# Performance work log

Measured on AMD Instinct MI355X. Metric: run time of the kernel, lower is better.

## Reference

```python
import jax, jax.numpy as jnp
import numpy as np

V, E, H, S, B, MAX_OOV = 50000, 256, 512, 500, 64, 50


def setup_inputs() -> dict:
    key = jax.random.key(0)
    ks = jax.random.split(key, 22)
    s = 0.02  # param init scale
    return {
        "input_token": jax.random.randint(ks[0], (B, 1), 0, V),
        "encoder_hidden_states": jax.random.normal(ks[1], (S, B, 2 * H), jnp.float32),
        "projected_encoder_hidden_states": jax.random.normal(ks[2], (S, B, H), jnp.float32),
        "src_mask": jnp.ones((B, S), dtype=bool),
        "prev_hidden": jax.random.normal(ks[3], (1, B, H), jnp.float32),
        "encoder_batch_extended_vocab": jax.random.randint(ks[4], (B, S), 0, V + MAX_OOV),
        "batch_max_oov": MAX_OOV,
        # learned parameters
        "emb": jax.random.normal(ks[5], (V, E), jnp.float32) * s,
        "attn_Wq": jax.random.normal(ks[6], (H, H), jnp.float32) * s,   # query_layer, no bias
        "attn_We": jax.random.normal(ks[7], (1, H), jnp.float32) * s,   # energy_layer, no bias
        "gru_Wih": jax.random.normal(ks[8], (3 * H, E + 2 * H), jnp.float32) * s,
        "gru_Whh": jax.random.normal(ks[9], (3 * H, H), jnp.float32) * s,
        "gru_bih": jax.random.normal(ks[10], (3 * H,), jnp.float32) * s,
        "gru_bhh": jax.random.normal(ks[11], (3 * H,), jnp.float32) * s,
        "lin_W": jax.random.normal(ks[12], (H, E + 3 * H), jnp.float32) * s,
        "lin_b": jax.random.normal(ks[13], (H,), jnp.float32) * s,
        "pg_W": jax.random.normal(ks[14], (1, E + 3 * H), jnp.float32) * s,
        "pg_b": jax.random.normal(ks[15], (1,), jnp.float32) * s,
        "out_W": jax.random.normal(ks[16], (V, H), jnp.float32) * s,
        "out_b": jax.random.normal(ks[17], (V,), jnp.float32) * s,
    }


def _forward(input_token, enc_h, proj_key, prev_hidden, ext_vocab, max_oov,
             emb, attn_Wq, attn_We, gru_Wih, gru_Whh, gru_bih, gru_bhh,
             lin_W, lin_b, pg_W, pg_b, out_W, out_b):
    b = input_token.shape[0]
    embed = jnp.transpose(emb[input_token], (1, 0, 2))  # [1,B,E]

    # Bahdanau attention (softmax over source dim 0; mask unused, as in source)
    q = jnp.einsum('tbh,oh->tbo', prev_hidden, attn_Wq)            # [1,B,H]
    scores = jnp.einsum('sbh,oh->sb', jnp.tanh(q + proj_key), attn_We)  # [S,B]
    alphas = jax.nn.softmax(scores, axis=0)                        # [S,B]
    context = jnp.einsum('sb,sbd->bd', alphas, enc_h)[None]        # [1,B,2H]
    attention_dist = alphas.T                                      # [B,S]

    # GRU cell (torch gate order: r, z, n)
    x = jnp.concatenate([embed, context], axis=2)[0]               # [B,E+2H]
    h = prev_hidden[0]                                             # [B,H]
    gi = x @ gru_Wih.T + gru_bih                                   # [B,3H]
    gh = h @ gru_Whh.T + gru_bhh
    i_r, i_z, i_n = jnp.split(gi, 3, axis=1)
    h_r, h_z, h_n = jnp.split(gh, 3, axis=1)
    r = jax.nn.sigmoid(i_r + h_r)
    z = jax.nn.sigmoid(i_z + h_z)
    n = jnp.tanh(i_n + r * h_n)
    h_new = (1.0 - z) * n + z * h                                  # [B,H]
    rnn_output = h_new[None]                                       # [1,B,H]

    concat = jnp.concatenate([embed, rnn_output, context], axis=2)  # [1,B,E+3H]
    p_gen = jax.nn.sigmoid(jnp.einsum('tbf,of->tbo', concat, pg_W) + pg_b)  # [1,B,1]
    lin = jnp.einsum('tbf,of->tbo', concat, lin_W) + lin_b          # [1,B,H]
    logits = jnp.einsum('tbh,vh->tbv', lin, out_W) + out_b          # [1,B,V]

    gen_prob = p_gen * jax.nn.softmax(logits, axis=2)               # [1,B,V]
    attn_prob = ((1.0 - p_gen) * attention_dist[None])[0]           # [B,S]

    ext = jnp.concatenate(
        [gen_prob, jnp.zeros((1, b, max_oov), gen_prob.dtype)], axis=2) + 1e-12  # [1,B,V+oov]
    rows = jnp.arange(b)[:, None]
    merged = ext.at[0, rows, ext_vocab].add(attn_prob)              # scatter_add over vocab dim
    output = jnp.log(merged)
    return output, h_new[None]


def reference(input_token, encoder_hidden_states, projected_encoder_hidden_states,
              src_mask, prev_hidden, encoder_batch_extended_vocab, batch_max_oov,
              emb, attn_Wq, attn_We, gru_Wih, gru_Whh, gru_bih, gru_bhh,
              lin_W, lin_b, pg_W, pg_b, out_W, out_b):
    return _forward(input_token, encoder_hidden_states, projected_encoder_hidden_states,
                    prev_hidden, encoder_batch_extended_vocab, batch_max_oov,
                    emb, attn_Wq, attn_We, gru_Wih, gru_Whh, gru_bih, gru_bhh,
                    lin_W, lin_b, pg_W, pg_b, out_W, out_b)
```

## Files before the change

kernel.cpp:

```cpp
#include <hip/hip_runtime.h>
#include <hip/hip_bf16.h>
#include <math.h>

namespace {
constexpr int V = 50000, E = 256, H = 512, S = 500, B = 64, OOVN = 50;
constexpr int VEXT = V + OOVN;
constexpr int CCAT = E + 3 * H;
constexpr int G3 = 3 * H;
constexpr int NLB = 391;

typedef __attribute__((ext_vector_type(8))) short short8;
typedef __attribute__((ext_vector_type(4))) float f32x4;

__device__ __forceinline__ float wsum(float v) {
#pragma unroll
  for (int off = 32; off > 0; off >>= 1) v += __shfl_xor(v, off, 64);
  return v;
}
__device__ __forceinline__ float sigmoidf(float x) { return 1.f / (1.f + __expf(-x)); }
__device__ __forceinline__ float fast_tanh(float x) {
  x = fminf(fmaxf(x, -15.f), 15.f);
  float e = __expf(2.f * x);
  return __fdividef(e - 1.f, e + 1.f);
}
__device__ __forceinline__ void smerge_s(float& m, float& l, float om, float ol) {
  float nm = fmaxf(m, om);
  if (nm == -INFINITY) { m = nm; return; }
  l = l * __expf(m - nm) + ol * __expf(om - nm);
  m = nm;
}

__device__ __forceinline__ short bf16_rn_s(float f) {
  __hip_bfloat16 h = __float2bfloat16(f);
  return __builtin_bit_cast(short, h);
}
__device__ __forceinline__ void hilo1(float f, short* hi, short* lo) {
  unsigned u = __float_as_uint(f);
  *hi = (short)(u >> 16);
  *lo = bf16_rn_s(f - __uint_as_float(u & 0xffff0000u));
}
__device__ __forceinline__ void hilo8(float4 a, float4 b, short8& hi, short8& lo) {
  float f[8] = {a.x, a.y, a.z, a.w, b.x, b.y, b.z, b.w};
#pragma unroll
  for (int i = 0; i < 8; ++i) {
    unsigned u = __float_as_uint(f[i]);
    hi[i] = (short)(u >> 16);
    lo[i] = bf16_rn_s(f[i] - __uint_as_float(u & 0xffff0000u));
  }
}

template <int KSTEPS>
__device__ __forceinline__ void gemm16(const short* __restrict__ Xhi,
                                       const short* __restrict__ Xlo, int ldx, int xk0,
                                       const float* __restrict__ W, int ldw, int wk0,
                                       int n0, float* __restrict__ C, int ldc) {
  const int l = threadIdx.x & 63;
  const int r16 = l & 15, q16 = l >> 4;
  f32x4 acc[4];
#pragma unroll
  for (int t = 0; t < 4; ++t) acc[t] = (f32x4){0.f, 0.f, 0.f, 0.f};

  const float* wp = W + (size_t)(n0 + r16) * ldw + wk0 + q16 * 8;
  const short* xh[4];
  const short* xl[4];
#pragma unroll
  for (int t = 0; t < 4; ++t) {
    int row = t * 16 + r16;
    xh[t] = Xhi + (size_t)row * ldx + xk0 + q16 * 8;
    xl[t] = Xlo + (size_t)row * ldx + xk0 + q16 * 8;
  }

#pragma unroll
  for (int ks = 0; ks < KSTEPS; ++ks) {
    const int ko = ks * 32;
    float4 w0 = *reinterpret_cast<const float4*>(wp + ko);
    float4 w1 = *reinterpret_cast<const float4*>(wp + ko + 4);
    short8 whi, wlo;
    hilo8(w0, w1, whi, wlo);
#pragma unroll
    for (int t = 0; t < 4; ++t) {
      short8 ah = *reinterpret_cast<const short8*>(xh[t] + ko);
      short8 al = *reinterpret_cast<const short8*>(xl[t] + ko);
      acc[t] = __builtin_amdgcn_mfma_f32_16x16x32_bf16(ah, whi, acc[t], 0, 0, 0);
      acc[t] = __builtin_amdgcn_mfma_f32_16x16x32_bf16(al, whi, acc[t], 0, 0, 0);
      acc[t] = __builtin_amdgcn_mfma_f32_16x16x32_bf16(ah, wlo, acc[t], 0, 0, 0);
    }
  }
#pragma unroll
  for (int t = 0; t < 4; ++t) {
#pragma unroll
    for (int r = 0; r < 4; ++r) {
      int row = t * 16 + q16 * 4 + r;
      C[(size_t)row * ldc + n0 + r16] = acc[t][r];
    }
  }
}

__global__ void k_prep(const int* __restrict__ tok, const float* __restrict__ emb,
                       const float* __restrict__ prevh, float* __restrict__ cc,
                       short* __restrict__ cch, short* __restrict__ ccl,
                       short* __restrict__ hh, short* __restrict__ hl) {
  int i = blockIdx.x * 256 + threadIdx.x;
  hilo1(prevh[i], &hh[i], &hl[i]);
  if (i < 16384) {
    int b = i >> 8, e = i & 255;
    float v = emb[(size_t)tok[b] * E + e];
    cc[b * CCAT + e] = v;
    hilo1(v, &cch[b * CCAT + e], &ccl[b * CCAT + e]);
  }
}

__global__ void __launch_bounds__(256) k_gemm_qgh(
    const short* __restrict__ hh, const short* __restrict__ hl,
    const float* __restrict__ Wq, const float* __restrict__ Whh,
    float* __restrict__ qpart, float* __restrict__ ghp) {
  int w = blockIdx.x * 4 + (threadIdx.x >> 6);
  if (w < 128) {
    int c = w >> 5, nt = w & 31;
    gemm16<4>(hh, hl, H, c * 128, Wq, H, c * 128, nt * 16,
              qpart + (size_t)c * 64 * H, H);
  } else {
    int w2 = w - 128;
    int c = w2 / 96, nt = w2 % 96;
    gemm16<8>(hh, hl, H, c * 256, Whh, H, c * 256, nt * 16,
              ghp + (size_t)c * 64 * G3, G3);
  }
}

__global__ void k_scores(const float* __restrict__ qpart, const float* __restrict__ pk,
                         const float* __restrict__ We, float* __restrict__ scores) {
  int lane = threadIdx.x & 63;
  int gw = blockIdx.x * 4 + (threadIdx.x >> 6);
  int s = gw >> 6, b = gw & 63;
  const float* q0 = qpart + b * H + lane * 8;
  const float* kr = pk + ((size_t)s * B + b) * H + lane * 8;
  const float* er = We + lane * 8;
  float part = 0.f;
#pragma unroll
  for (int i = 0; i < 2; ++i) {
    float4 qa = *reinterpret_cast<const float4*>(q0 + i * 4);
    float4 qb = *reinterpret_cast<const float4*>(q0 + 64 * H + i * 4);
    float4 qc = *reinterpret_cast<const float4*>(q0 + 128 * H + i * 4);
    float4 qd = *reinterpret_cast<const float4*>(q0 + 192 * H + i * 4);
    float4 kv = *reinterpret_cast<const float4*>(kr + i * 4);
    float4 ev = *reinterpret_cast<const float4*>(er + i * 4);
    part += fast_tanh(qa.x + qb.x + qc.x + qd.x + kv.x) * ev.x +
            fast_tanh(qa.y + qb.y + qc.y + qd.y + kv.y) * ev.y +
            fast_tanh(qa.z + qb.z + qc.z + qd.z + kv.z) * ev.z +
            fast_tanh(qa.w + qb.w + qc.w + qd.w + kv.w) * ev.w;
  }
  part = wsum(part);
  if (lane == 0) scores[s * B + b] = part;
}

__global__ void k_softmax_s(const float* __restrict__ scores, float* __restrict__ alphasT) {
  int b = blockIdx.x, t = threadIdx.x;
  int w = t >> 6, lane = t & 63;
  __shared__ float rm[8], rl[8];
  float v = (t < S) ? scores[t * B + b] : -INFINITY;
  float m = v;
#pragma unroll
  for (int off = 32; off > 0; off >>= 1) m = fmaxf(m, __shfl_xor(m, off, 64));
  if (lane == 0) rm[w] = m;
  __syncthreads();
  float bm = rm[0];
#pragma unroll
  for (int i = 1; i < 8; ++i) bm = fmaxf(bm, rm[i]);
  float e = (t < S) ? __expf(v - bm) : 0.f;
  float sw = wsum(e);
  if (lane == 0) rl[w] = sw;
  __syncthreads();
  float tot = rl[0];
#pragma unroll
  for (int i = 1; i < 8; ++i) tot += rl[i];
  if (t < S) alphasT[b * S + t] = e / tot;
}

__global__ void k_ctx(const float* __restrict__ alphasT, const float* __restrict__ ench,
                      float* __restrict__ ctxp) {
  int b = blockIdx.x, chf = blockIdx.y, sh = blockIdx.z;
  int t = threadIdx.x;
  __shared__ float sa[250];
  if (t < 250) sa[t] = alphasT[b * S + sh * 250 + t];
  __syncthreads();
  const float* base = ench + ((size_t)(sh * 250) * B + b) * 1024 + chf * 512 + t;
  float a0 = 0.f, a1 = 0.f;
#pragma unroll 8
  for (int s = 0; s < 250; s += 2) {
    a0 += sa[s] * base[(size_t)s * (B * 1024)];
    a1 += sa[s + 1] * base[(size_t)(s + 1) * (B * 1024)];
  }
  ctxp[((sh * B + b) * 1024) + chf * 512 + t] = a0 + a1;
}

__global__ void k_ctx2(const float* __restrict__ ctxp, float* __restrict__ cc,
                       short* __restrict__ cch, short* __restrict__ ccl) {
  int b = blockIdx.x, t = threadIdx.x;
  int c = t * 4;
  float4 v0 = *reinterpret_cast<const float4*>(&ctxp[(b * 1024) + c]);
  float4 v1 = *reinterpret_cast<const float4*>(&ctxp[((B + b) * 1024) + c]);
  float r[4] = {v0.x + v1.x, v0.y + v1.y, v0.z + v1.z, v0.w + v1.w};
#pragma unroll
  for (int i = 0; i < 4; ++i) {
    int col = 768 + c + i;
    cc[b * CCAT + col] = r[i];
    hilo1(r[i], &cch[b * CCAT + col], &ccl[b * CCAT + col]);
  }
}

__global__ void __launch_bounds__(256) k_gemm_big(
    const short* __restrict__ cch, const short* __restrict__ ccl,
    const float* __restrict__ Wih, const float* __restrict__ linW,
    float* __restrict__ gip, float* __restrict__ linpart) {
  int w = blockIdx.x * 4 + (threadIdx.x >> 6);
  if (w < 480) {
    int c = w / 96, nt = w % 96;
    int xk0 = (c == 0) ? 0 : 768 + (c - 1) * 256;
    int wk0 = c * 256;
    gemm16<8>(cch, ccl, CCAT, xk0, Wih, 1280, wk0, nt * 16,
              gip + (size_t)c * 64 * G3, G3);
  } else {
    int w2 = w - 480;
    int c = w2 >> 5, nt = w2 & 31;
    int k0 = (c == 0) ? 0 : 768 + (c - 1) * 256;
    gemm16<8>(cch, ccl, CCAT, k0, linW, CCAT, k0, nt * 16,
              linpart + (size_t)c * 64 * H, H);
  }
}

__global__ void k_gates(const float* __restrict__ gip, const float* __restrict__ ghp,
                        const float* __restrict__ bih, const float* __restrict__ bhh,
                        const float* __restrict__ prevh, const float* __restrict__ pgW,
                        const float* __restrict__ pgb, float* __restrict__ cc,
                        short* __restrict__ cch, short* __restrict__ ccl,
                        float* __restrict__ hout, float* __restrict__ pgsum) {
  int b = blockIdx.x, j = threadIdx.x;
  float ir = bih[j], iz = bih[512 + j], in_ = bih[1024 + j];
#pragma unroll
  for (int c = 0; c < 5; ++c) {
    const float* g = gip + (size_t)c * 64 * G3 + b * G3;
    ir += g[j]; iz += g[512 + j]; in_ += g[1024 + j];
  }
  float hr = bhh[j], hz = bhh[512 + j], hn = bhh[1024 + j];
#pragma unroll
  for (int c = 0; c < 2; ++c) {
    const float* g = ghp + (size_t)c * 64 * G3 + b * G3;
    hr += g[j]; hz += g[512 + j]; hn += g[1024 + j];
  }
  float r = sigmoidf(ir + hr);
  float z = sigmoidf(iz + hz);
  float n = fast_tanh(in_ + r * hn);
  float h = prevh[b * H + j];
  float hnew = (1.f - z) * n + z * h;
  hout[b * H + j] = hnew;
  cc[b * CCAT + E + j] = hnew;
  hilo1(hnew, &cch[b * CCAT + E + j], &ccl[b * CCAT + E + j]);
  float acc = hnew * pgW[E + j];
  acc += cc[b * CCAT + 768 + j] * pgW[768 + j];
  acc += cc[b * CCAT + 1280 + j] * pgW[1280 + j];
  if (j < 256) acc += cc[b * CCAT + j] * pgW[j];
  acc = wsum(acc);
  __shared__ float sl[8];
  int w = j >> 6, lane = j & 63;
  if (lane == 0) sl[w] = acc;
  __syncthreads();
  if (j == 0) {
    float tot = pgb[0];
#pragma unroll
    for (int i = 0; i < 8; ++i) tot += sl[i];
    pgsum[b] = tot;
  }
}

__global__ void __launch_bounds__(256) k_gemm_linh(const short* __restrict__ cch,
                                                   const short* __restrict__ ccl,
                                                   const float* __restrict__ linW,
                                                   float* __restrict__ linpart) {
  int w = blockIdx.x * 4 + (threadIdx.x >> 6);
  int c = w >> 5, nt = w & 31;
  int k0 = 256 + c * 256;
  gemm16<8>(cch, ccl, CCAT, k0, linW, CCAT, k0, nt * 16,
            linpart + (size_t)(5 + c) * 64 * H, H);
}

__global__ void k_linfin(const float* __restrict__ linpart, const float* __restrict__ linb,
                         short* __restrict__ lh) {
  int idx = blockIdx.x * 256 + threadIdx.x;
  int b = idx >> 9, o = idx & 511;
  float v = linb[o];
#pragma unroll
  for (int c = 0; c < 7; ++c) v += linpart[(size_t)c * 64 * H + b * H + o];
  lh[idx] = bf16_rn_s(v);
}

__global__ void __launch_bounds__(512) k_gemm_logits(
    const short* __restrict__ lh, const float* __restrict__ outW,
    const float* __restrict__ outb, float* __restrict__ logits,
    float* __restrict__ pm, float* __restrict__ pl) {
  __shared__ __align__(16) short xs[64 * 512];
  __shared__ float pml[8][64][2];
  char* xb = reinterpret_cast<char*>(xs);
  int tid = threadIdx.x;
#pragma unroll
  for (int k = 0; k < 8; ++k) {
    int m = k * 512 + tid;
    int row = m >> 6;
    short8 v = *reinterpret_cast<const short8*>(lh + (size_t)m * 8);
    int byte = (m * 16) ^ ((row & 7) << 4);
    *reinterpret_cast<short8*>(xb + byte) = v;
  }
  __syncthreads();
  const int l = tid & 63;
  const int r16 = l & 15, q16 = l >> 4;
  const int wid = tid >> 6;
  const int waveId = blockIdx.x * 8 + wid;
  const bool active = waveId < V / 16;
  if (active) {
    const int n0 = waveId * 16;
    f32x4 acc[4];
#pragma unroll
    for (int t = 0; t < 4; ++t) acc[t] = (f32x4){0.f, 0.f, 0.f, 0.f};
    const float* wp = outW + (size_t)(n0 + r16) * H + q16 * 8;
    int arow[4], aswz[4];
#pragma unroll
    for (int t = 0; t < 4; ++t) {
      int row = t * 16 + r16;
      arow[t] = row * 1024 + q16 * 16;
      aswz[t] = (row & 7) << 4;
    }
#pragma unroll
    for (int ks = 0; ks < 16; ++ks) {
      float4 w0 = *reinterpret_cast<const float4*>(wp + ks * 32);
      float4 w1 = *reinterpret_cast<const float4*>(wp + ks * 32 + 4);
      short8 wh;
      wh[0] = bf16_rn_s(w0.x); wh[1] = bf16_rn_s(w0.y);
      wh[2] = bf16_rn_s(w0.z); wh[3] = bf16_rn_s(w0.w);
      wh[4] = bf16_rn_s(w1.x); wh[5] = bf16_rn_s(w1.y);
      wh[6] = bf16_rn_s(w1.z); wh[7] = bf16_rn_s(w1.w);
#pragma unroll
      for (int t = 0; t < 4; ++t) {
        short8 a = *reinterpret_cast<const short8*>(xb + ((arow[t] + ks * 64) ^ aswz[t]));
        acc[t] = __builtin_amdgcn_mfma_f32_16x16x32_bf16(a, wh, acc[t], 0, 0, 0);
      }
    }
    float bv = outb[n0 + r16];
#pragma unroll
    for (int t = 0; t < 4; ++t) {
#pragma unroll
      for (int r = 0; r < 4; ++r) {
        float y = acc[t][r] + bv;
        int row = t * 16 + q16 * 4 + r;
        logits[(size_t)row * V + n0 + r16] = y;
        float m = y;
#pragma unroll
        for (int off = 8; off > 0; off >>= 1) m = fmaxf(m, __shfl_xor(m, off, 64));
        float e = __expf(y - m);
#pragma unroll
        for (int off = 8; off > 0; off >>= 1) e += __shfl_xor(e, off, 64);
        if (r16 == 0) { pml[wid][row][0] = m; pml[wid][row][1] = e; }
      }
    }
  } else if (r16 == 0) {
#pragma unroll
    for (int t = 0; t < 4; ++t)
#pragma unroll
      for (int r = 0; r < 4; ++r) {
        int row = t * 16 + q16 * 4 + r;
        pml[wid][row][0] = -INFINITY;
        pml[wid][row][1] = 0.f;
      }
  }
  __syncthreads();
  if (tid < 64) {
    float m = pml[0][tid][0], lv = pml[0][tid][1];
#pragma unroll
    for (int i = 1; i < 8; ++i) smerge_s(m, lv, pml[i][tid][0], pml[i][tid][1]);
    pm[blockIdx.x * 64 + tid] = m;
    pl[blockIdx.x * 64 + tid] = lv;
  }
}

__global__ void k_final(const float* __restrict__ logits, const float* __restrict__ pm,
                        const float* __restrict__ pl, const float* __restrict__ pgsum,
                        const int* __restrict__ extv, const float* __restrict__ alphasT,
                        float* __restrict__ out) {
  int b = blockIdx.x, c = blockIdx.y, t = threadIdx.x;
  __shared__ float sp_[5056];
  __shared__ float rm[4], rl[4];
  float m = -INFINITY, lv = 0.f;
  for (int i = t; i < NLB; i += 256) smerge_s(m, lv, pm[i * 64 + b], pl[i * 64 + b]);
#pragma unroll
  for (int off = 32; off > 0; off >>= 1) {
    float om = __shfl_xor(m, off, 64), ol = __shfl_xor(lv, off, 64);
    smerge_s(m, lv, om, ol);
  }
  int w = t >> 6, lane = t & 63;
  if (lane == 0) { rm[w] = m; rl[w] = lv; }
  __syncthreads();
  m = rm[0]; lv = rl[0];
#pragma unroll
  for (int i = 1; i < 4; ++i) smerge_s(m, lv, rm[i], rl[i]);
  float pg = sigmoidf(pgsum[b]);
  float scale = pg / lv;
  const int base = c * 5000;
  const int len = (c == 9) ? 5050 : 5000;
  const float* lr = logits + (size_t)b * V + base;
  for (int i = t; i < len; i += 256)
    sp_[i] = (i < 5000) ? scale * __expf(lr[i] - m) + 1e-12f : 1e-12f;
  __syncthreads();
  float wgt = 1.f - pg;
  for (int s = t; s < S; s += 256) {
    int idx = extv[b * S + s] - base;
    if ((unsigned)idx < (unsigned)len) atomicAdd(&sp_[idx], wgt * alphasT[b * S + s]);
  }
  __syncthreads();
  float* orow = out + (size_t)b * VEXT + base;
  for (int i = t; i < len; i += 256) orow[i] = logf(sp_[i]);
}
}

extern "C" void kernel_launch(void* const* d_in, const int* in_sizes, int n_in,
                              void* d_out, int out_size, void* d_ws, size_t ws_size,
                              hipStream_t stream) {
  const int*   tok   = (const int*)d_in[0];
  const float* ench  = (const float*)d_in[1];
  const float* pk    = (const float*)d_in[2];
  const float* prevh = (const float*)d_in[4];
  const int*   extv  = (const int*)d_in[5];
  const float* emb   = (const float*)d_in[7];
  const float* Wq    = (const float*)d_in[8];
  const float* We    = (const float*)d_in[9];
  const float* Wih   = (const float*)d_in[10];
  const float* Whh   = (const float*)d_in[11];
  const float* bih   = (const float*)d_in[12];
  const float* bhh   = (const float*)d_in[13];
  const float* linW  = (const float*)d_in[14];
  const float* linb  = (const float*)d_in[15];
  const float* pgW   = (const float*)d_in[16];
  const float* pgb   = (const float*)d_in[17];
  const float* outW  = (const float*)d_in[18];
  const float* outb  = (const float*)d_in[19];

  float* out = (float*)d_out;
  float* ws = (float*)d_ws;

  float* qpart   = ws;
  float* scores  = qpart + 131072;
  float* alphasT = scores + 32000;
  float* ctxp    = alphasT + 32000;
  float* cc      = ctxp + 131072;
  float* gip     = cc + 114688;
  float* ghp     = gip + 491520;
  float* linpart = ghp + 196608;
  float* pgsum   = linpart + 229376;
  float* logits  = pgsum + 64;
  float* pm      = logits + 3200000;
  float* pl      = pm + 25024;
  short* sp      = (short*)(pl + 25024);
  short* cch = sp;
  short* ccl = cch + 114688;
  short* hh  = ccl + 114688;
  short* hl  = hh + 32768;
  short* lh  = hl + 32768;
  float* hout = out + (size_t)B * VEXT;

  k_prep<<<dim3(128), dim3(256), 0, stream>>>(tok, emb, prevh, cc, cch, ccl, hh, hl);
  k_gemm_qgh<<<dim3(80), dim3(256), 0, stream>>>(hh, hl, Wq, Whh, qpart, ghp);
  k_scores<<<dim3(8000), dim3(256), 0, stream>>>(qpart, pk, We, scores);
  k_softmax_s<<<dim3(B), dim3(512), 0, stream>>>(scores, alphasT);
  k_ctx<<<dim3(64, 2, 2), dim3(512), 0, stream>>>(alphasT, ench, ctxp);
  k_ctx2<<<dim3(B), dim3(256), 0, stream>>>(ctxp, cc, cch, ccl);
  k_gemm_big<<<dim3(160), dim3(256), 0, stream>>>(cch, ccl, Wih, linW, gip, linpart);
  k_gates<<<dim3(B), dim3(512), 0, stream>>>(gip, ghp, bih, bhh, prevh, pgW, pgb, cc, cch,
                                             ccl, hout, pgsum);
  k_gemm_linh<<<dim3(16), dim3(256), 0, stream>>>(cch, ccl, linW, linpart);
  k_linfin<<<dim3(128), dim3(256), 0, stream>>>(linpart, linb, lh);
  k_gemm_logits<<<dim3(NLB), dim3(512), 0, stream>>>(lh, outW, outb, logits, pm, pl);
  k_final<<<dim3(B, 10), dim3(256), 0, stream>>>(logits, pm, pl, pgsum, extv, alphasT, out);
}
```

Baseline: 162.8 us.

## Fuse all decoder phases into one cooperative persistent kernel with grid syncs

Replaces the chain of twelve kernel launches with a single cooperative kernel that runs each phase as a grid-stride loop separated by grid-wide barriers. Launch gaps and per-kernel tail effects are the cost it targets. It also regroups work: context reduction is split into four source chunks, and the linear-layer hidden-part GEMM appears to be folded into a later phase. A fallback path of per-phase kernels remains. Risks include grid barrier overhead, lower occupancy from the 68KB shared buffer and 512-thread blocks, and host-side occupancy and property queries on every call.

Result: slower. 531.9 us (+226.7%).

```diff
diff --git a/kernel.cpp b/kernel.cpp
--- a/kernel.cpp
+++ b/kernel.cpp
@@ -1,6 +1,9 @@
 #include <hip/hip_runtime.h>
 #include <hip/hip_bf16.h>
+#include <hip/hip_cooperative_groups.h>
 #include <math.h>
+
+namespace cg = cooperative_groups;
 
 namespace {
 constexpr int V = 50000, E = 256, H = 512, S = 500, B = 64, OOVN = 50;
@@ -8,9 +11,22 @@
 constexpr int CCAT = E + 3 * H;
 constexpr int G3 = 3 * H;
 constexpr int NLB = 391;
+constexpr int SMEM_BYTES = 69632;
 
 typedef __attribute__((ext_vector_type(8))) short short8;
 typedef __attribute__((ext_vector_type(4))) float f32x4;
+
+struct P {
+  const int* tok; const float* ench; const float* pk; const float* prevh;
+  const int* extv; const float* emb; const float* Wq; const float* We;
+  const float* Wih; const float* Whh; const float* bih; const float* bhh;
+  const float* linW; const float* linb; const float* pgW; const float* pgb;
+  const float* outW; const float* outb;
+  float* out; float* qpart; float* scores; float* alphasT; float* ctxp;
+  float* cc; float* gip; float* ghp; float* linpart; float* pgsum;
+  float* logits; float* pm; float* pl; float* hout;
+  short* cch; short* ccl; short* hh; short* hl; short* lh;
+};
 
 __device__ __forceinline__ float wsum(float v) {
 #pragma unroll
@@ -29,7 +45,6 @@
   l = l * __expf(m - nm) + ol * __expf(om - nm);
   m = nm;
 }
-
 __device__ __forceinline__ short bf16_rn_s(float f) {
   __hip_bfloat16 h = __float2bfloat16(f);
   return __builtin_bit_cast(short, h);
@@ -50,16 +65,14 @@
 }
 
 template <int KSTEPS>
-__device__ __forceinline__ void gemm16(const short* __restrict__ Xhi,
-                                       const short* __restrict__ Xlo, int ldx, int xk0,
-                                       const float* __restrict__ W, int ldw, int wk0,
-                                       int n0, float* __restrict__ C, int ldc) {
+__device__ __forceinline__ void gemm_core(const short* __restrict__ Xhi,
+                                          const short* __restrict__ Xlo, int ldx, int xk0,
+                                          const float* __restrict__ W, int ldw, int wk0,
+                                          int n0, f32x4 acc[4]) {
   const int l = threadIdx.x & 63;
   const int r16 = l & 15, q16 = l >> 4;
-  f32x4 acc[4];
 #pragma unroll
   for (int t = 0; t < 4; ++t) acc[t] = (f32x4){0.f, 0.f, 0.f, 0.f};
-
   const float* wp = W + (size_t)(n0 + r16) * ldw + wk0 + q16 * 8;
   const short* xh[4];
   const short* xl[4];
@@ -69,7 +82,6 @@
     xh[t] = Xhi + (size_t)row * ldx + xk0 + q16 * 8;
     xl[t] = Xlo + (size_t)row * ldx + xk0 + q16 * 8;
   }
-
 #pragma unroll
   for (int ks = 0; ks < KSTEPS; ++ks) {
     const int ko = ks * 32;
@@ -86,395 +98,461 @@
       acc[t] = __builtin_amdgcn_mfma_f32_16x16x32_bf16(ah, wlo, acc[t], 0, 0, 0);
     }
   }
-#pragma unroll
-  for (int t = 0; t < 4; ++t) {
+}
+template <int KSTEPS>
+__device__ __forceinline__ void gemm_store(const short* Xhi, const short* Xlo, int ldx,
+                                           int xk0, const float* W, int ldw, int wk0,
+                                           int n0, float* C, int ldc) {
+  f32x4 acc[4];
+  gemm_core<KSTEPS>(Xhi, Xlo, ldx, xk0, W, ldw, wk0, n0, acc);
+  const int l = threadIdx.x & 63;
+  const int r16 = l & 15, q16 = l >> 4;
+#pragma unroll
+  for (int t = 0; t < 4; ++t)
 #pragma unroll
     for (int r = 0; r < 4; ++r) {
       int row = t * 16 + q16 * 4 + r;
       C[(size_t)row * ldc + n0 + r16] = acc[t][r];
     }
-  }
-}
-
-__global__ void k_prep(const int* __restrict__ tok, const float* __restrict__ emb,
-                       const float* __restrict__ prevh, float* __restrict__ cc,
-                       short* __restrict__ cch, short* __restrict__ ccl,
-                       short* __restrict__ hh, short* __restrict__ hl) {
-  int i = blockIdx.x * 256 + threadIdx.x;
-  hilo1(prevh[i], &hh[i], &hl[i]);
-  if (i < 16384) {
-    int b = i >> 8, e = i & 255;
-    float v = emb[(size_t)tok[b] * E + e];
-    cc[b * CCAT + e] = v;
-    hilo1(v, &cch[b * CCAT + e], &ccl[b * CCAT + e]);
-  }
-}
-
-__global__ void __launch_bounds__(256) k_gemm_qgh(
-    const short* __restrict__ hh, const short* __restrict__ hl,
-    const float* __restrict__ Wq, const float* __restrict__ Whh,
-    float* __restrict__ qpart, float* __restrict__ ghp) {
-  int w = blockIdx.x * 4 + (threadIdx.x >> 6);
-  if (w < 128) {
-    int c = w >> 5, nt = w & 31;
-    gemm16<4>(hh, hl, H, c * 128, Wq, H, c * 128, nt * 16,
-              qpart + (size_t)c * 64 * H, H);
-  } else {
-    int w2 = w - 128;
-    int c = w2 / 96, nt = w2 % 96;
-    gemm16<8>(hh, hl, H, c * 256, Whh, H, c * 256, nt * 16,
-              ghp + (size_t)c * 64 * G3, G3);
-  }
-}
-
-__global__ void k_scores(const float* __restrict__ qpart, const float* __restrict__ pk,
-                         const float* __restrict__ We, float* __restrict__ scores) {
+}
+
+
+__device__ void ph_prep(const P& p) {
+  for (int i = blockIdx.x * blockDim.x + threadIdx.x; i < B * H;
+       i += gridDim.x * blockDim.x) {
+    hilo1(p.prevh[i], &p.hh[i], &p.hl[i]);
+    if (i < B * E) {
+      int b = i >> 8, e = i & 255;
+      float v = p.emb[(size_t)p.tok[b] * E + e];
+      p.cc[b * CCAT + e] = v;
+      hilo1(v, &p.cch[b * CCAT + e], &p.ccl[b * CCAT + e]);
+    }
+  }
+}
+
+__device__ void ph_qgh(const P& p) {
+  int W = gridDim.x * (blockDim.x >> 6);
+  for (int w = blockIdx.x * (blockDim.x >> 6) + (threadIdx.x >> 6); w < 320; w += W) {
+    if (w < 128) {
+      int c = w >> 5, nt = w & 31;
+      gemm_store<4>(p.hh, p.hl, H, c * 128, p.Wq, H, c * 128, nt * 16,
+                    p.qpart + (size_t)c * 64 * H, H);
+    } else {
+      int w2 = w - 128;
+      int c = w2 / 96, nt = w2 % 96;
+      gemm_store<8>(p.hh, p.hl, H, c * 256, p.Whh, H, c * 256, nt * 16,
+                    p.ghp + (size_t)c * 64 * G3, G3);
+    }
+  }
+}
+
+__device__ void ph_scores(const P& p) {
   int lane = threadIdx.x & 63;
-  int gw = blockIdx.x * 4 + (threadIdx.x >> 6);
-  int s = gw >> 6, b = gw & 63;
-  const float* q0 = qpart + b * H + lane * 8;
-  const float* kr = pk + ((size_t)s * B + b) * H + lane * 8;
-  const float* er = We + lane * 8;
-  float part = 0.f;
-#pragma unroll
-  for (int i = 0; i < 2; ++i) {
-    float4 qa = *reinterpret_cast<const float4*>(q0 + i * 4);
-    float4 qb = *reinterpret_cast<const float4*>(q0 + 64 * H + i * 4);
-    float4 qc = *reinterpret_cast<const float4*>(q0 + 128 * H + i * 4);
-    float4 qd = *reinterpret_cast<const float4*>(q0 + 192 * H + i * 4);
-    float4 kv = *reinterpret_cast<const float4*>(kr + i * 4);
-    float4 ev = *reinterpret_cast<const float4*>(er + i * 4);
-    part += fast_tanh(qa.x + qb.x + qc.x + qd.x + kv.x) * ev.x +
-            fast_tanh(qa.y + qb.y + qc.y + qd.y + kv.y) * ev.y +
-            fast_tanh(qa.z + qb.z + qc.z + qd.z + kv.z) * ev.z +
-            fast_tanh(qa.w + qb.w + qc.w + qd.w + kv.w) * ev.w;
-  }
-  part = wsum(part);
-  if (lane == 0) scores[s * B + b] = part;
-}
-
-__global__ void k_softmax_s(const float* __restrict__ scores, float* __restrict__ alphasT) {
-  int b = blockIdx.x, t = threadIdx.x;
-  int w = t >> 6, lane = t & 63;
-  __shared__ float rm[8], rl[8];
-  float v = (t < S) ? scores[t * B + b] : -INFINITY;
-  float m = v;
-#pragma unroll
-  for (int off = 32; off > 0; off >>= 1) m = fmaxf(m, __shfl_xor(m, off, 64));
-  if (lane == 0) rm[w] = m;
-  __syncthreads();
-  float bm = rm[0];
-#pragma unroll
-  for (int i = 1; i < 8; ++i) bm = fmaxf(bm, rm[i]);
-  float e = (t < S) ? __expf(v - bm) : 0.f;
-  float sw = wsum(e);
-  if (lane == 0) rl[w] = sw;
-  __syncthreads();
-  float tot = rl[0];
-#pragma unroll
-  for (int i = 1; i < 8; ++i) tot += rl[i];
-  if (t < S) alphasT[b * S + t] = e / tot;
-}
-
-__global__ void k_ctx(const float* __restrict__ alphasT, const float* __restrict__ ench,
-                      float* __restrict__ ctxp) {
-  int b = blockIdx.x, chf = blockIdx.y, sh = blockIdx.z;
+  int W = gridDim.x * (blockDim.x >> 6);
+  for (int gw = blockIdx.x * (blockDim.x >> 6) + (threadIdx.x >> 6); gw < S * B; gw += W) {
+    int s = gw >> 6, b = gw & 63;
+    const float* q0 = p.qpart + b * H + lane * 8;
+    const float* kr = p.pk + ((size_t)s * B + b) * H + lane * 8;
+    const float* er = p.We + lane * 8;
+    float part = 0.f;
+#pragma unroll
+    for (int i = 0; i < 2; ++i) {
+      float4 qa = *reinterpret_cast<const float4*>(q0 + i * 4);
+      float4 qb = *reinterpret_cast<const float4*>(q0 + 64 * H + i * 4);
+      float4 qc = *reinterpret_cast<const float4*>(q0 + 128 * H + i * 4);
+      float4 qd = *reinterpret_cast<const float4*>(q0 + 192 * H + i * 4);
+      float4 kv = *reinterpret_cast<const float4*>(kr + i * 4);
+      float4 ev = *reinterpret_cast<const float4*>(er + i * 4);
+      part += fast_tanh(qa.x + qb.x + qc.x + qd.x + kv.x) * ev.x +
+              fast_tanh(qa.y + qb.y + qc.y + qd.y + kv.y) * ev.y +
+              fast_tanh(qa.z + qb.z + qc.z + qd.z + kv.z) * ev.z +
+              fast_tanh(qa.w + qb.w + qc.w + qd.w + kv.w) * ev.w;
+    }
+    part = wsum(part);
+    if (lane == 0) p.scores[s * B + b] = part;
+  }
+}
+
+__device__ void ph_softmax(const P& p, char* smem) {
+  float* rm = (float*)smem;
+  float* rl = rm + 8;
+  int t = threadIdx.x, w = t >> 6, lane = t & 63;
+  for (int b = blockIdx.x; b < B; b += gridDim.x) {
+    __syncthreads();
+    float v = (t < S) ? p.scores[t * B + b] : -INFINITY;
+    float m = v;
+#pragma unroll
+    for (int off = 32; off > 0; off >>= 1) m = fmaxf(m, __shfl_xor(m, off, 64));
+    if (lane == 0) rm[w] = m;
+    __syncthreads();
+    float bm = rm[0];
+#pragma unroll
+    for (int i = 1; i < 8; ++i) bm = fmaxf(bm, rm[i]);
+    float e = (t < S) ? __expf(v - bm) : 0.f;
+    float sw = wsum(e);
+    if (lane == 0) rl[w] = sw;
+    __syncthreads();
+    float tot = rl[0];
+#pragma unroll
+    for (int i = 1; i < 8; ++i) tot += rl[i];
+    if (t < S) p.alphasT[b * S + t] = e / tot;
+  }
+}
+
+__device__ void ph_ctx(const P& p, char* smem) {
+  float* sa = (float*)smem;
   int t = threadIdx.x;
-  __shared__ float sa[250];
-  if (t < 250) sa[t] = alphasT[b * S + sh * 250 + t];
-  __syncthreads();
-  const float* base = ench + ((size_t)(sh * 250) * B + b) * 1024 + chf * 512 + t;
-  float a0 = 0.f, a1 = 0.f;
-#pragma unroll 8
-  for (int s = 0; s < 250; s += 2) {
-    a0 += sa[s] * base[(size_t)s * (B * 1024)];
-    a1 += sa[s + 1] * base[(size_t)(s + 1) * (B * 1024)];
-  }
-  ctxp[((sh * B + b) * 1024) + chf * 512 + t] = a0 + a1;
-}
-
-__global__ void k_ctx2(const float* __restrict__ ctxp, float* __restrict__ cc,
-                       short* __restrict__ cch, short* __restrict__ ccl) {
-  int b = blockIdx.x, t = threadIdx.x;
-  int c = t * 4;
-  float4 v0 = *reinterpret_cast<const float4*>(&ctxp[(b * 1024) + c]);
-  float4 v1 = *reinterpret_cast<const float4*>(&ctxp[((B + b) * 1024) + c]);
-  float r[4] = {v0.x + v1.x, v0.y + v1.y, v0.z + v1.z, v0.w + v1.w};
-#pragma unroll
-  for (int i = 0; i < 4; ++i) {
-    int col = 768 + c + i;
-    cc[b * CCAT + col] = r[i];
-    hilo1(r[i], &cch[b * CCAT + col], &ccl[b * CCAT + col]);
-  }
-}
-
-__global__ void __launch_bounds__(256) k_gemm_big(
-    const short* __restrict__ cch, const short* __restrict__ ccl,
-    const float* __restrict__ Wih, const float* __restrict__ linW,
-    float* __restrict__ gip, float* __restrict__ linpart) {
-  int w = blockIdx.x * 4 + (threadIdx.x >> 6);
-  if (w < 480) {
-    int c = w / 96, nt = w % 96;
-    int xk0 = (c == 0) ? 0 : 768 + (c - 1) * 256;
-    int wk0 = c * 256;
-    gemm16<8>(cch, ccl, CCAT, xk0, Wih, 1280, wk0, nt * 16,
-              gip + (size_t)c * 64 * G3, G3);
-  } else {
-    int w2 = w - 480;
-    int c = w2 >> 5, nt = w2 & 31;
-    int k0 = (c == 0) ? 0 : 768 + (c - 1) * 256;
-    gemm16<8>(cch, ccl, CCAT, k0, linW, CCAT, k0, nt * 16,
-              linpart + (size_t)c * 64 * H, H);
-  }
-}
-
-__global__ void k_gates(const float* __restrict__ gip, const float* __restrict__ ghp,
-                        const float* __restrict__ bih, const float* __restrict__ bhh,
-                        const float* __restrict__ prevh, const float* __restrict__ pgW,
-                        const float* __restrict__ pgb, float* __restrict__ cc,
-                        short* __restrict__ cch, short* __restrict__ ccl,
-                        float* __restrict__ hout, float* __restrict__ pgsum) {
-  int b = blockIdx.x, j = threadIdx.x;
-  float ir = bih[j], iz = bih[512 + j], in_ = bih[1024 + j];
-#pragma unroll
-  for (int c = 0; c < 5; ++c) {
-    const float* g = gip + (size_t)c * 64 * G3 + b * G3;
-    ir += g[j]; iz += g[512 + j]; in_ += g[1024 + j];
-  }
-  float hr = bhh[j], hz = bhh[512 + j], hn = bhh[1024 + j];
-#pragma unroll
-  for (int c = 0; c < 2; ++c) {
-    const float* g = ghp + (size_t)c * 64 * G3 + b * G3;
-    hr += g[j]; hz += g[512 + j]; hn += g[1024 + j];
-  }
-  float r = sigmoidf(ir + hr);
-  float z = sigmoidf(iz + hz);
-  float n = fast_tanh(in_ + r * hn);
-  float h = prevh[b * H + j];
-  float hnew = (1.f - z) * n + z * h;
-  hout[b * H + j] = hnew;
-  cc[b * CCAT + E + j] = hnew;
-  hilo1(hnew, &cch[b * CCAT + E + j], &ccl[b * CCAT + E + j]);
-  float acc = hnew * pgW[E + j];
-  acc += cc[b * CCAT + 768 + j] * pgW[768 + j];
-  acc += cc[b * CCAT + 1280 + j] * pgW[1280 + j];
-  if (j < 256) acc += cc[b * CCAT + j] * pgW[j];
-  acc = wsum(acc);
-  __shared__ float sl[8];
+  for (int it = blockIdx.x; it < 512; it += gridDim.x) {
+    int b = it >> 3, chf = (it >> 2) & 1, sh = it & 3;
+    __syncthreads();
+    if (t < 125) sa[t] = p.alphasT[b * S + sh * 125 + t];
+    __syncthreads();
+    const float* base = p.ench + ((size_t)(sh * 125) * B + b) * 1024 + chf * 512 + t;
+    float a0 = 0.f, a1 = 0.f;
+#pragma unroll 5
+    for (int s = 0; s < 124; s += 2) {
+      a0 += sa[s] * base[(size_t)s * (B * 1024)];
+      a1 += sa[s + 1] * base[(size_t)(s + 1) * (B * 1024)];
+    }
+    a0 += sa[124] * base[(size_t)124 * (B * 1024)];
+    p.ctxp[((sh * B + b) * 1024) + chf * 512 + t] = a0 + a1;
+  }
+}
+
+__device__ void ph_ctx2(const P& p) {
+  for (int i = blockIdx.x * blockDim.x + threadIdx.x; i < B * 1024;
+       i += gridDim.x * blockDim.x) {
+    int b = i >> 10, col = i & 1023;
+    float v = p.ctxp[(b)*1024 + col] + p.ctxp[(B + b) * 1024 + col] +
+              p.ctxp[(2 * B + b) * 1024 + col] + p.ctxp[(3 * B + b) * 1024 + col];
+    int cix = b * CCAT + 768 + col;
+    p.cc[cix] = v;
+    hilo1(v, &p.cch[cix], &p.ccl[cix]);
+  }
+}
+
+__device__ void ph_big(const P& p) {
+  int W = gridDim.x * (blockDim.x >> 6);
+  for (int w = blockIdx.x * (blockDim.x >> 6) + (threadIdx.x >> 6); w < 640; w += W) {
+    if (w < 480) {
+      int c = w / 96, nt = w % 96;
+      int xk0 = (c == 0) ? 0 : 768 + (c - 1) * 256;
+      gemm_store<8>(p.cch, p.ccl, CCAT, xk0, p.Wih, 1280, c * 256, nt * 16,
+                    p.gip + (size_t)c * 64 * G3, G3);
+    } else {
+      int w2 = w - 480;
+      int c = w2 >> 5, nt = w2 & 31;
+      int k0 = (c == 0) ? 0 : 768 + (c - 1) * 256;
+      gemm_store<8>(p.cch, p.ccl, CCAT, k0, p.linW, CCAT, k0, nt * 16,
+                    p.linpart + (size_t)c * 64 * H, H);
+    }
+  }
+}
+
+__device__ void ph_gates(const P& p, char* smem) {
+  float* sl = (float*)smem;
+  int j = threadIdx.x;
   int w = j >> 6, lane = j & 63;
-  if (lane == 0) sl[w] = acc;
-  __syncthreads();
-  if (j == 0) {
-    float tot = pgb[0];
-#pragma unroll
-    for (int i = 0; i < 8; ++i) tot += sl[i];
-    pgsum[b] = tot;
-  }
-}
-
-__global__ void __launch_bounds__(256) k_gemm_linh(const short* __restrict__ cch,
-                                                   const short* __restrict__ ccl,
-                                                   const float* __restrict__ linW,
-                                                   float* __restrict__ linpart) {
-  int w = blockIdx.x * 4 + (threadIdx.x >> 6);
-  int c = w >> 5, nt = w & 31;
-  int k0 = 256 + c * 256;
-  gemm16<8>(cch, ccl, CCAT, k0, linW, CCAT, k0, nt * 16,
-            linpart + (size_t)(5 + c) * 64 * H, H);
-}
-
-__global__ void k_linfin(const float* __restrict__ linpart, const float* __restrict__ linb,
-                         short* __restrict__ lh) {
-  int idx = blockIdx.x * 256 + threadIdx.x;
-  int b = idx >> 9, o = idx & 511;
-  float v = linb[o];
-#pragma unroll
-  for (int c = 0; c < 7; ++c) v += linpart[(size_t)c * 64 * H + b * H + o];
-  lh[idx] = bf16_rn_s(v);
-}
-
-__global__ void __launch_bounds__(512) k_gemm_logits(
-    const short* __restrict__ lh, const float* __restrict__ outW,
-    const float* __restrict__ outb, float* __restrict__ logits,
-    float* __restrict__ pm, float* __restrict__ pl) {
-  __shared__ __align__(16) short xs[64 * 512];
-  __shared__ float pml[8][64][2];
-  char* xb = reinterpret_cast<char*>(xs);
+  for (int b = blockIdx.x; b < B; b += gridDim.x) {
+    __syncthreads();
+    float ir = p.bih[j], iz = p.bih[512 + j], in_ = p.bih[1024 + j];
+#pragma unroll
+    for (int c = 0; c < 5; ++c) {
+      const float* g = p.gip + (size_t)c * 64 * G3 + b * G3;
+      ir += g[j]; iz += g[512 + j]; in_ += g[1024 + j];
+    }
+    float hr = p.bhh[j], hz = p.bhh[512 + j], hn = p.bhh[1024 + j];
+#pragma unroll
+    for (int c = 0; c < 2; ++c) {
+      const float* g = p.ghp + (size_t)c * 64 * G3 + b * G3;
+      hr += g[j]; hz += g[512 + j]; hn += g[1024 + j];
+    }
+    float r = sigmoidf(ir + hr);
+    float z = sigmoidf(iz + hz);
+    float n = fast_tanh(in_ + r * hn);
+    float h = p.prevh[b * H + j];
+    float hnew = (1.f - z) * n + z * h;
+    p.hout[b * H + j] = hnew;
+    p.cc[b * CCAT + E + j] = hnew;
+    hilo1(hnew, &p.cch[b * CCAT + E + j], &p.ccl[b * CCAT + E + j]);
+    float acc = hnew * p.pgW[E + j];
+    acc += p.cc[b * CCAT + 768 + j] * p.pgW[768 + j];
+    acc += p.cc[b * CCAT + 1280 + j] * p.pgW[1280 + j];
+    if (j < 256) acc += p.cc[b * CCAT + j] * p.pgW[j];
+    acc = wsum(acc);
+    if (lane == 0) sl[w] = acc;
+    __syncthreads();
+    if (j == 0) {
+      float tot = p.pgb[0];
+#pragma unroll
+      for (int i = 0; i < 8; ++i) tot += sl[i];
+      p.pgsum[b] = tot;
+    }
+  }
+}
+
+__device__ void ph_linfin(const P& p) {
+  int W = gridDim.x * (blockDim.x >> 6);
+  for (int w = blockIdx.x * (blockDim.x >> 6) + (threadIdx.x >> 6); w < 32; w += W) {
+    f32x4 acc[4];
+    gemm_core<16>(p.cch, p.ccl, CCAT, 256, p.linW, CCAT, 256, w * 16, acc);
+    const int l = threadIdx.x & 63;
+    const int r16 = l & 15, q16 = l >> 4;
+    int col = w * 16 + r16;
+    float bv = p.linb[col];
+#pragma unroll
+    for (int t = 0; t < 4; ++t)
+#pragma unroll
+      for (int r = 0; r < 4; ++r) {
+        int row = t * 16 + q16 * 4 + r;
+        float v = acc[t][r] + bv;
+#pragma unroll
+        for (int c = 0; c < 5; ++c) v += p.linpart[(size_t)c * 64 * H + row * H + col];
+        p.lh[row * H + col] = bf16_rn_s(v);
+      }
+  }
+}
+
+__device__ void ph_logits(const P& p, char* smem) {
+  char* xb = smem;
+  float (*pml)[64][2] = (float(*)[64][2])(smem + 65536);
   int tid = threadIdx.x;
+  const int l = tid & 63, r16 = l & 15, q16 = l >> 4, wid = tid >> 6;
 #pragma unroll
   for (int k = 0; k < 8; ++k) {
     int m = k * 512 + tid;
     int row = m >> 6;
-    short8 v = *reinterpret_cast<const short8*>(lh + (size_t)m * 8);
+    short8 v = *reinterpret_cast<const short8*>(p.lh + (size_t)m * 8);
     int byte = (m * 16) ^ ((row & 7) << 4);
     *reinterpret_cast<short8*>(xb + byte) = v;
   }
+  int arow[4], aswz[4];
+#pragma unroll
+  for (int t = 0; t < 4; ++t) {
+    int row = t * 16 + r16;
+    arow[t] = row * 1024 + q16 * 16;
+    aswz[t] = (row & 7) << 4;
+  }
   __syncthreads();
-  const int l = tid & 63;
-  const int r16 = l & 15, q16 = l >> 4;
-  const int wid = tid >> 6;
-  const int waveId = blockIdx.x * 8 + wid;
-  const bool active = waveId < V / 16;
-  if (active) {
-    const int n0 = waveId * 16;
-    f32x4 acc[4];
-#pragma unroll
-    for (int t = 0; t < 4; ++t) acc[t] = (f32x4){0.f, 0.f, 0.f, 0.f};
-    const float* wp = outW + (size_t)(n0 + r16) * H + q16 * 8;
-    int arow[4], aswz[4];
-#pragma unroll
-    for (int t = 0; t < 4; ++t) {
-      int row = t * 16 + r16;
-      arow[t] = row * 1024 + q16 * 16;
-      aswz[t] = (row & 7) << 4;
-    }
-#pragma unroll
-    for (int ks = 0; ks < 16; ++ks) {
-      float4 w0 = *reinterpret_cast<const float4*>(wp + ks * 32);
-      float4 w1 = *reinterpret_cast<const float4*>(wp + ks * 32 + 4);
-      short8 wh;
-      wh[0] = bf16_rn_s(w0.x); wh[1] = bf16_rn_s(w0.y);
-      wh[2] = bf16_rn_s(w0.z); wh[3] = bf16_rn_s(w0.w);
-      wh[4] = bf16_rn_s(w1.x); wh[5] = bf16_rn_s(w1.y);
-      wh[6] = bf16_rn_s(w1.z); wh[7] = bf16_rn_s(w1.w);
-#pragma unroll
-      for (int t = 0; t < 4; ++t) {
-        short8 a = *reinterpret_cast<const short8*>(xb + ((arow[t] + ks * 64) ^ aswz[t]));
-        acc[t] = __builtin_amdgcn_mfma_f32_16x16x32_bf16(a, wh, acc[t], 0, 0, 0);
+  for (int vb = blockIdx.x; vb < NLB; vb += gridDim.x) {
+    int tile = vb * 8 + wid;
+    if (tile < V / 16) {
+      const int n0 = tile * 16;
+      f32x4 acc[4];
+#pragma unroll
+      for (int t = 0; t < 4; ++t) acc[t] = (f32x4){0.f, 0.f, 0.f, 0.f};
+      const float* wp = p.outW + (size_t)(n0 + r16) * H + q16 * 8;
+#pragma unroll
+      for (int ks = 0; ks < 16; ++ks) {
+        float4 w0 = *reinterpret_cast<const float4*>(wp + ks * 32);
+        float4 w1 = *reinterpret_cast<const float4*>(wp + ks * 32 + 4);
+        short8 wh;
+        wh[0] = bf16_rn_s(w0.x); wh[1] = bf16_rn_s(w0.y);
+        wh[2] = bf16_rn_s(w0.z); wh[3] = bf16_rn_s(w0.w);
+        wh[4] = bf16_rn_s(w1.x); wh[5] = bf16_rn_s(w1.y);
+        wh[6] = bf16_rn_s(w1.z); wh[7] = bf16_rn_s(w1.w);
+#pragma unroll
+        for (int t = 0; t < 4; ++t) {
+          short8 a = *reinterpret_cast<const short8*>(xb + ((arow[t] + ks * 64) ^ aswz[t]));
+          acc[t] = __builtin_amdgcn_mfma_f32_16x16x32_bf16(a, wh, acc[t], 0, 0, 0);
+        }
       }
-    }
-    float bv = outb[n0 + r16];
-#pragma unroll
-    for (int t = 0; t < 4; ++t) {
-#pragma unroll
-      for (int r = 0; r < 4; ++r) {
-        float y = acc[t][r] + bv;
-        int row = t * 16 + q16 * 4 + r;
-        logits[(size_t)row * V + n0 + r16] = y;
-        float m = y;
-#pragma unroll
-        for (int off = 8; off > 0; off >>= 1) m = fmaxf(m, __shfl_xor(m, off, 64));
-        float e = __expf(y - m);
-#pragma unroll
-        for (int off = 8; off > 0; off >>= 1) e += __shfl_xor(e, off, 64);
-        if (r16 == 0) { pml[wid][row][0] = m; pml[wid][row][1] = e; }
-      }
-    }
-  } else if (r16 == 0) {
-#pragma unroll
-    for (int t = 0; t < 4; ++t)
-#pragma unroll
-      for (int r = 0; r < 4; ++r) {
-        int row = t * 16 + q16 * 4 + r;
-        pml[wid][row][0] = -INFINITY;
-        pml[wid][row][1] = 0.f;
-      }
-  }
-  __syncthreads();
-  if (tid < 64) {
-    float m = pml[0][tid][0], lv = pml[0][tid][1];
-#pragma unroll
-    for (int i = 1; i < 8; ++i) smerge_s(m, lv, pml[i][tid][0], pml[i][tid][1]);
-    pm[blockIdx.x * 64 + tid] = m;
-    pl[blockIdx.x * 64 + tid] = lv;
-  }
-}
-
-__global__ void k_final(const float* __restrict__ logits, const float* __restrict__ pm,
-                        const float* __restrict__ pl, const float* __restrict__ pgsum,
-                        const int* __restrict__ extv, const float* __restrict__ alphasT,
-                        float* __restrict__ out) {
-  int b = blockIdx.x, c = blockIdx.y, t = threadIdx.x;
-  __shared__ float sp_[5056];
-  __shared__ float rm[4], rl[4];
-  float m = -INFINITY, lv = 0.f;
-  for (int i = t; i < NLB; i += 256) smerge_s(m, lv, pm[i * 64 + b], pl[i * 64 + b]);
-#pragma unroll
-  for (int off = 32; off > 0; off >>= 1) {
-    float om = __shfl_xor(m, off, 64), ol = __shfl_xor(lv, off, 64);
-    smerge_s(m, lv, om, ol);
-  }
-  int w = t >> 6, lane = t & 63;
-  if (lane == 0) { rm[w] = m; rl[w] = lv; }
-  __syncthreads();
-  m = rm[0]; lv = rl[0];
-#pragma unroll
-  for (int i = 1; i < 4; ++i) smerge_s(m, lv, rm[i], rl[i]);
-  float pg = sigmoidf(pgsum[b]);
-  float scale = pg / lv;
-  const int base = c * 5000;
-  const int len = (c == 9) ? 5050 : 5000;
-  const float* lr = logits + (size_t)b * V + base;
-  for (int i = t; i < len; i += 256)
-    sp_[i] = (i < 5000) ? scale * __expf(lr[i] - m) + 1e-12f : 1e-12f;
-  __syncthreads();
-  float wgt = 1.f - pg;
-  for (int s = t; s < S; s += 256) {
-    int idx = extv[b * S + s] - base;
-    if ((unsigned)idx < (unsigned)len) atomicAdd(&sp_[idx], wgt * alphasT[b * S + s]);
-  }
-  __syncthreads();
-  float* orow = out + (size_t)b * VEXT + base;
-  for (int i = t; i < len; i += 256) orow[i] = logf(sp_[i]);
+      float bv = p.outb[n0 + r16];
+#pragma unroll
+      for (int t = 0; t < 4; ++t)
+#pragma unroll
+        for (int r = 0; r < 4; ++r) {
+          float y = acc[t][r] + bv;
+          int row = t * 16 + q16 * 4 + r;
+          p.logits[(size_t)row * V + n0 + r16] = y;
+          float m = y;
+#pragma unroll
+          for (int off = 8; off > 0; off >>= 1) m = fmaxf(m, __shfl_xor(m, off, 64));
+          float e = __expf(y - m);
+#pragma unroll
+          for (int off = 8; off > 0; off >>= 1) e += __shfl_xor(e, off, 64);
+          if (r16 == 0) { pml[wid][row][0] = m; pml[wid][row][1] = e; }
+        }
+    } else if (r16 == 0) {
+#pragma unroll
+      for (int t = 0; t < 4; ++t)
+#pragma unroll
+        for (int r = 0; r < 4; ++r) {
+          int row = t * 16 + q16 * 4 + r;
+          pml[wid][row][0] = -INFINITY;
+          pml[wid][row][1] = 0.f;
+        }
+    }
+    __syncthreads();
+    if (tid < 64) {
+      float m = pml[0][tid][0], lv = pml[0][tid][1];
+#pragma unroll
+      for (int i = 1; i < 8; ++i) smerge_s(m, lv, pml[i][tid][0], pml[i][tid][1]);
+      p.pm[vb * 64 + tid] = m;
+      p.pl[vb * 64 + tid] = lv;
+    }
+    __syncthreads();
+  }
+}
+
+__device__ void ph_final(const P& p, char* smem) {
+  float* sp_ = (float*)smem;
+  float* rr = (float*)(smem + 20224);
+  float* rl2 = rr + 8;
+  int t = threadIdx.x, w = t >> 6, lane = t & 63;
+  for (int it = blockIdx.x; it < 640; it += gridDim.x) {
+    int b = it & 63, c = it >> 6;
+    float m = -INFINITY, lv = 0.f;
+    if (t < NLB) { m = p.pm[t * 64 + b]; lv = p.pl[t * 64 + b]; }
+#pragma unroll
+    for (int off = 32; off > 0; off >>= 1) {
+      float om = __shfl_xor(m, off, 64), ol = __shfl_xor(lv, off, 64);
+      smerge_s(m, lv, om, ol);
+    }
+    if (lane == 0) { rr[w] = m; rl2[w] = lv; }
+    __syncthreads();
+    m = rr[0]; lv = rl2[0];
+#pragma unroll
+    for (int i = 1; i < 8; ++i) smerge_s(m, lv, rr[i], rl2[i]);
+    float pg = sigmoidf(p.pgsum[b]);
+    float scale = pg / lv;
+    const int base = c * 5000;
+    const int len = (c == 9) ? 5050 : 5000;
+    const float* lr = p.logits + (size_t)b * V + base;
+    for (int i = t; i < len; i += 512)
+      sp_[i] = (i < 5000) ? scale * __expf(lr[i] - m) + 1e-12f : 1e-12f;
+    __syncthreads();
+    float wgt = 1.f - pg;
+    for (int s = t; s < S; s += 512) {
+      int idx = p.extv[b * S + s] - base;
+      if ((unsigned)idx < (unsigned)len) atomicAdd(&sp_[idx], wgt * p.alphasT[b * S + s]);
+    }
+    __syncthreads();
+    float* orow = p.out + (size_t)b * VEXT + base;
+    for (int i = t; i < len; i += 512) orow[i] = __logf(sp_[i]);
+    __syncthreads();
+  }
+}
+
+__global__ void __launch_bounds__(512, 4) k_mega(P p) {
+  __shared__ __align__(16) char smem[SMEM_BYTES];
+  cg::grid_group g = cg::this_grid();
+  ph_prep(p);          g.sync();
+  ph_qgh(p);           g.sync();
+  ph_scores(p);        g.sync();
+  ph_softmax(p, smem); g.sync();
+  ph_ctx(p, smem);     g.sync();
+  ph_ctx2(p);          g.sync();
+  ph_big(p);           g.sync();
+  ph_gates(p, smem);   g.sync();
+  ph_linfin(p);        g.sync();
+  ph_logits(p, smem);  g.sync();
+  ph_final(p, smem);
+}
+
+__global__ void __launch_bounds__(512) k_p0(P p) { ph_prep(p); }
+__global__ void __launch_bounds__(512) k_p1(P p) { ph_qgh(p); }
+__global__ void __launch_bounds__(512) k_p2(P p) { ph_scores(p); }
+__global__ void __launch_bounds__(512) k_p3(P p) {
+  __shared__ __align__(16) char smem[64];
+  ph_softmax(p, smem);
+}
+__global__ void __launch_bounds__(512) k_p4(P p) {
+  __shared__ __align__(16) char smem[512];
+  ph_ctx(p, smem);
+}
+__global__ void __launch_bounds__(512) k_p5(P p) { ph_ctx2(p); }
+__global__ void __launch_bounds__(512) k_p6(P p) { ph_big(p); }
+__global__ void __launch_bounds__(512) k_p7(P p) {
+  __shared__ __align__(16) char smem[64];
+  ph_gates(p, smem);
+}
+__global__ void __launch_bounds__(512) k_p8(P p) { ph_linfin(p); }
+__global__ void __launch_bounds__(512) k_p9(P p) {
+  __shared__ __align__(16) char smem[SMEM_BYTES];
+  ph_logits(p, smem);
+}
+__global__ void __launch_bounds__(512) k_p10(P p) {
+  __shared__ __align__(16) char smem[20304];
+  ph_final(p, smem);
 }
 }
 
 extern "C" void kernel_launch(void* const* d_in, const int* in_sizes, int n_in,
                               void* d_out, int out_size, void* d_ws, size_t ws_size,
                               hipStream_t stream) {
-  const int*   tok   = (const int*)d_in[0];
-  const float* ench  = (const float*)d_in[1];
-  const float* pk    = (const float*)d_in[2];
-  const float* prevh = (const float*)d_in[4];
-  const int*   extv  = (const int*)d_in[5];
-  const float* emb   = (const float*)d_in[7];
-  const float* Wq    = (const float*)d_in[8];
-  const float* We    = (const float*)d_in[9];
-  const float* Wih   = (const float*)d_in[10];
-  const float* Whh   = (const float*)d_in[11];
-  const float* bih   = (const float*)d_in[12];
-  const float* bhh   = (const float*)d_in[13];
-  const float* linW  = (const float*)d_in[14];
-  const float* linb  = (const float*)d_in[15];
-  const float* pgW   = (const float*)d_in[16];
-  const float* pgb   = (const float*)d_in[17];
-  const float* outW  = (const float*)d_in[18];
-  const float* outb  = (const float*)d_in[19];
-
-  float* out = (float*)d_out;
+  P p;
+  p.tok   = (const int*)d_in[0];
+  p.ench  = (const float*)d_in[1];
+  p.pk    = (const float*)d_in[2];
+  p.prevh = (const float*)d_in[4];
+  p.extv  = (const int*)d_in[5];
+  p.emb   = (const float*)d_in[7];
+  p.Wq    = (const float*)d_in[8];
+  p.We    = (const float*)d_in[9];
+  p.Wih   = (const float*)d_in[10];
+  p.Whh   = (const float*)d_in[11];
+  p.bih   = (const float*)d_in[12];
+  p.bhh   = (const float*)d_in[13];
+  p.linW  = (const float*)d_in[14];
+  p.linb  = (const float*)d_in[15];
+  p.pgW   = (const float*)d_in[16];
+  p.pgb   = (const float*)d_in[17];
+  p.outW  = (const float*)d_in[18];
+  p.outb  = (const float*)d_in[19];
+  p.out   = (float*)d_out;
+
   float* ws = (float*)d_ws;
-
-  float* qpart   = ws;
-  float* scores  = qpart + 131072;
-  float* alphasT = scores + 32000;
-  float* ctxp    = alphasT + 32000;
-  float* cc      = ctxp + 131072;
-  float* gip     = cc + 114688;
-  float* ghp     = gip + 491520;
-  float* linpart = ghp + 196608;
-  float* pgsum   = linpart + 229376;
-  float* logits  = pgsum + 64;
-  float* pm      = logits + 3200000;
-  float* pl      = pm + 25024;
-  short* sp      = (short*)(pl + 25024);
-  short* cch = sp;
-  short* ccl = cch + 114688;
-  short* hh  = ccl + 114688;
-  short* hl  = hh + 32768;
-  short* lh  = hl + 32768;
-  float* hout = out + (size_t)B * VEXT;
-
-  k_prep<<<dim3(128), dim3(256), 0, stream>>>(tok, emb, prevh, cc, cch, ccl, hh, hl);
-  k_gemm_qgh<<<dim3(80), dim3(256), 0, stream>>>(hh, hl, Wq, Whh, qpart, ghp);
-  k_scores<<<dim3(8000), dim3(256), 0, stream>>>(qpart, pk, We, scores);
-  k_softmax_s<<<dim3(B), dim3(512), 0, stream>>>(scores, alphasT);
-  k_ctx<<<dim3(64, 2, 2), dim3(512), 0, stream>>>(alphasT, ench, ctxp);
-  k_ctx2<<<dim3(B), dim3(256), 0, stream>>>(ctxp, cc, cch, ccl);
-  k_gemm_big<<<dim3(160), dim3(256), 0, stream>>>(cch, ccl, Wih, linW, gip, linpart);
-  k_gates<<<dim3(B), dim3(512), 0, stream>>>(gip, ghp, bih, bhh, prevh, pgW, pgb, cc, cch,
-                                             ccl, hout, pgsum);
-  k_gemm_linh<<<dim3(16), dim3(256), 0, stream>>>(cch, ccl, linW, linpart);
-  k_linfin<<<dim3(128), dim3(256), 0, stream>>>(linpart, linb, lh);
-  k_gemm_logits<<<dim3(NLB), dim3(512), 0, stream>>>(lh, outW, outb, logits, pm, pl);
-  k_final<<<dim3(B, 10), dim3(256), 0, stream>>>(logits, pm, pl, pgsum, extv, alphasT, out);
-}
+  p.qpart   = ws;
+  p.scores  = p.qpart + 131072;
+  p.alphasT = p.scores + 32000;
+  p.ctxp    = p.alphasT + 32000;
+  p.cc      = p.ctxp + 262144;
+  p.gip     = p.cc + 114688;
+  p.ghp     = p.gip + 491520;
+  p.linpart = p.ghp + 196608;
+  p.pgsum   = p.linpart + 163840;
+  p.logits  = p.pgsum + 64;
+  p.pm      = p.logits + 3200000;
+  p.pl      = p.pm + 25024;
+  short* sp = (short*)(p.pl + 25024);
+  p.cch = sp;
+  p.ccl = p.cch + 114688;
+  p.hh  = p.ccl + 114688;
+  p.hl  = p.hh + 32768;
+  p.lh  = p.hl + 32768;
+  p.hout = p.out + (size_t)B * VEXT;
+
+  bool launched = false;
+  int occ = 0;
+  hipError_t oe =
+      hipOccupancyMaxActiveBlocksPerMultiprocessor(&occ, (const void*)k_mega, 512, 0);
+  if (oe == hipSuccess && occ > 0) {
+    int devId = 0;
+    hipGetDevice(&devId);
+    hipDeviceProp_t prop;
+    if (hipGetDeviceProperties(&prop, devId) == hipSuccess) {
+      int nb = occ * prop.multiProcessorCount;
+      if (nb > 512) nb = 512;
+      if (nb >= 64) {
+        void* args[] = {(void*)&p};
+        hipError_t rc = hipLaunchCooperativeKernel((const void*)k_mega, dim3(nb),
+                                                   dim3(512), args, 0, stream);
+        launched = (rc == hipSuccess);
+      }
+    }
+  }
+  if (!launched) {
+    k_p0<<<dim3(64), dim3(512), 0, stream>>>(p);
+    k_p1<<<dim3(40), dim3(512), 0, stream>>>(p);
+    k_p2<<<dim3(4000), dim3(512), 0, stream>>>(p);
+    k_p3<<<dim3(64), dim3(512), 0, stream>>>(p);
+    k_p4<<<dim3(512), dim3(512), 0, stream>>>(p);
+    k_p5<<<dim3(128), dim3(512), 0, stream>>>(p);
+    k_p6<<<dim3(80), dim3(512), 0, stream>>>(p);
+    k_p7<<<dim3(64), dim3(512), 0, stream>>>(p);
+    k_p8<<<dim3(4), dim3(512), 0, stream>>>(p);
+    k_p9<<<dim3(391), dim3(512), 0, stream>>>(p);
+    k_p10<<<dim3(640), dim3(512), 0, stream>>>(p);
+  }
+}
```
